# Kernel tuning notes

Hardware: AMD Instinct MI355X
Metric: run time of the kernel (lower is better)

The kernel has to match this reference:

```python
import jax, jax.numpy as jnp
import numpy as np

B, N, D_NET = 16, 2048, 64
L_SFC, D_VNF = 16, 32
HID, NHEAD, DFF, NLAYERS = 128, 4, 8, 2
NUM_NODES = 1024
SEQ = L_SFC + 2
EPS = 1e-5


def setup_inputs() -> dict:
    key = jax.random.key(0)
    ks = iter(jax.random.split(key, 40))
    def nrm(shape, scale=0.02):
        return (jax.random.normal(next(ks), shape, dtype=jnp.float32) * scale)
    inp = {
        'net_state': jax.random.normal(next(ks), (B, N, D_NET), dtype=jnp.float32),
        'sfc_state': jax.random.normal(next(ks), (B, L_SFC, D_VNF), dtype=jnp.float32),
        'node_pair': jax.random.randint(next(ks), (B, 2), 0, NUM_NODES),
        # manual attention projections (torch Linear layout [out,in])
        'Wq': nrm((4 * D_NET, D_NET)), 'bq': jnp.zeros((4 * D_NET,), jnp.float32),
        'Wk': nrm((4 * D_NET, D_NET)), 'bk': jnp.zeros((4 * D_NET,), jnp.float32),
        'Wv': nrm((4 * D_NET, D_NET)), 'bv': jnp.zeros((4 * D_NET,), jnp.float32),
        'net_W': nrm((HID, 4 * D_NET)), 'net_b': jnp.zeros((HID,), jnp.float32),
        'node_embed': nrm((NUM_NODES, D_VNF), 1.0),
        'sfc_W': nrm((HID, D_VNF)), 'sfc_b': jnp.zeros((HID,), jnp.float32),
        'pos_embed': nrm((SEQ, HID), 1.0),
        # 2 TransformerEncoderLayers, stacked on leading axis
        'qkv_w': nrm((NLAYERS, 3 * HID, HID)), 'qkv_b': jnp.zeros((NLAYERS, 3 * HID), jnp.float32),
        'out_w': nrm((NLAYERS, HID, HID)), 'out_b': jnp.zeros((NLAYERS, HID), jnp.float32),
        'ln1_w': jnp.ones((NLAYERS, HID), jnp.float32), 'ln1_b': jnp.zeros((NLAYERS, HID), jnp.float32),
        'lin1_w': nrm((NLAYERS, DFF, HID)), 'lin1_b': jnp.zeros((NLAYERS, DFF), jnp.float32),
        'lin2_w': nrm((NLAYERS, HID, DFF)), 'lin2_b': jnp.zeros((NLAYERS, HID), jnp.float32),
        'ln2_w': jnp.ones((NLAYERS, HID), jnp.float32), 'ln2_b': jnp.zeros((NLAYERS, HID), jnp.float32),
    }
    return inp


def _layernorm(x, w, b):
    mu = jnp.mean(x, axis=-1, keepdims=True)
    var = jnp.mean(jnp.square(x - mu), axis=-1, keepdims=True)
    return (x - mu) * jax.lax.rsqrt(var + EPS) * w + b


def _mha(x, w_qkv, b_qkv, w_out, b_out, pad_mask):
    Bx, S, H = x.shape
    hd = H // NHEAD
    qkv = x @ w_qkv.T + b_qkv                      # [B,S,3H]
    q, k, v = jnp.split(qkv, 3, axis=-1)
    q = q.reshape(Bx, S, NHEAD, hd).transpose(0, 2, 1, 3)
    k = k.reshape(Bx, S, NHEAD, hd).transpose(0, 2, 1, 3)
    v = v.reshape(Bx, S, NHEAD, hd).transpose(0, 2, 1, 3)
    scores = jnp.einsum('bhqd,bhkd->bhqk', q, k) / jnp.float32(hd) ** 0.5
    scores = scores + jnp.where(pad_mask[:, None, None, :], -1e9, 0.0)
    attn = jax.nn.softmax(scores, axis=-1)
    o = jnp.einsum('bhqk,bhkd->bhqd', attn, v).transpose(0, 2, 1, 3).reshape(Bx, S, H)
    return o @ w_out.T + b_out


def reference(net_state, sfc_state, node_pair, Wq, bq, Wk, bk, Wv, bv,
              net_W, net_b, node_embed, sfc_W, sfc_b, pos_embed,
              qkv_w, qkv_b, out_w, out_b, ln1_w, ln1_b,
              lin1_w, lin1_b, lin2_w, lin2_b, ln2_w, ln2_b):
    # --- net branch: manual single-head self-attention over nodes ---
    Q = net_state @ Wq.T + bq                       # [B,N,4D]
    K = net_state @ Wk.T + bk
    V = net_state @ Wv.T + bv
    scores = jnp.einsum('bnd,bmd->bnm', Q, K) / jnp.float32(net_state.shape[-1]) ** 0.5
    net_out = jax.nn.softmax(scores, axis=-1) @ V   # [B,N,4D]
    net_out = net_out @ net_W.T + net_b             # [B,N,HID]
    # --- sfc branch ---
    pair_emb = node_embed[node_pair]                # [B,2,D_VNF]
    sfc = jnp.concatenate([pair_emb[:, :1], sfc_state, pair_emb[:, 1:2]], axis=1)
    pad_mask = jnp.sum(jnp.abs(sfc), axis=-1) == 0  # [B,SEQ]
    x = sfc @ sfc_W.T + sfc_b + pos_embed[None, :sfc.shape[1]]
    for l in range(NLAYERS):  # post-norm TransformerEncoderLayer, relu, dropout=0
        x = _layernorm(x + _mha(x, qkv_w[l], qkv_b[l], out_w[l], out_b[l], pad_mask), ln1_w[l], ln1_b[l])
        ff = jax.nn.relu(x @ lin1_w[l].T + lin1_b[l]) @ lin2_w[l].T + lin2_b[l]
        x = _layernorm(x + ff, ln2_w[l], ln2_b[l])
    return jnp.concatenate([net_out, x], axis=1)    # [B, N+SEQ, HID]
```

## Files before the change

### kernel.cpp

```cpp
#include <hip/hip_runtime.h>
#include <cstdint>
#include <cstddef>

#define B_   16
#define N_   2048
#define DN   64
#define DQ   256
#define HID_ 128
#define SEQ_ 18
#define OUTR 2066
#define KVB  32

typedef __attribute__((ext_vector_type(4)))  float f32x4;
typedef __attribute__((ext_vector_type(16))) float f32x16;
typedef __attribute__((ext_vector_type(8)))  short bf16x8;

__device__ __forceinline__ unsigned cvtpk(float lo, float hi) {
  unsigned w;
  asm("v_cvt_pk_bf16_f32 %0, %1, %2" : "=v"(w) : "v"(lo), "v"(hi));
  return w;
}
__device__ __forceinline__ short f2bf(float f) {
  union { float f; unsigned u; } v; v.f = f;
  unsigned r = v.u + 0x7fffu + ((v.u >> 16) & 1u);
  return (short)(r >> 16);
}
__device__ __forceinline__ bf16x8 cvt8(const float* p) {
  f32x4 a = *(const f32x4*)p, b = *(const f32x4*)(p + 4);
  union { unsigned u[4]; bf16x8 v; } r;
  r.u[0] = cvtpk(a[0], a[1]); r.u[1] = cvtpk(a[2], a[3]);
  r.u[2] = cvtpk(b[0], b[1]); r.u[3] = cvtpk(b[2], b[3]);
  return r.v;
}
__device__ __forceinline__ float hadd4(f32x4 v) { return (v[0] + v[1]) + (v[2] + v[3]); }

__device__ __forceinline__ bf16x8 mkfrag(unsigned wa, unsigned wb,
                                         unsigned wc, unsigned wd, bool hi) {
  unsigned sa = (unsigned)__shfl_xor((int)wa, 32);
  unsigned sb = (unsigned)__shfl_xor((int)wb, 32);
  unsigned sc = (unsigned)__shfl_xor((int)wc, 32);
  unsigned sd = (unsigned)__shfl_xor((int)wd, 32);
  union { unsigned u[4]; bf16x8 v; } r;
  r.u[0] = hi ? sc : wa;
  r.u[1] = hi ? sd : wb;
  r.u[2] = hi ? wc : sa;
  r.u[3] = hi ? wd : sb;
  return r.v;
}

__global__ __launch_bounds__(512) void proj_kernel(
    const float* __restrict__ net, const float* __restrict__ Wq, const float* __restrict__ bq,
    const float* __restrict__ Wk, const float* __restrict__ bk,
    const float* __restrict__ Wv, const float* __restrict__ bv,
    const float* __restrict__ netW,
    short* __restrict__ Qb, short* __restrict__ Kb, short* __restrict__ Gf) {
  __shared__ char psm[98304];
  short* wl = (short*)psm;
  char* vrm = psm + 32768;

  const int gid = blockIdx.x;
  const int b = gid >> 4;
  const int r0 = (gid & 15) * 128;
  const int t = threadIdx.x;
  const int w = t >> 6, lane = t & 63, ln = lane & 15, g = lane >> 4;
  const int rw = r0 + w * 16;
  const int xk = (ln & 7) << 4;

  bf16x8 af[2];
#pragma unroll
  for (int c = 0; c < 2; ++c)
    af[c] = cvt8(net + ((size_t)b * N_ + rw + ln) * DN + c * 32 + g * 8);

  const float* Ws[3] = {Wq, Wk, Wv};
  for (int m = 0; m < 3; ++m) {
    __syncthreads();
#pragma unroll
    for (int it = 0; it < 8; ++it) {
      int idx = it * 512 + t;
      int row = idx >> 4, c8 = idx & 15;
      f32x4 v = *(const f32x4*)(Ws[m] + row * 64 + c8 * 4);
      int byo = row * 128 + ((c8 * 8) ^ ((row & 7) << 4));
      *(uint2*)((char*)wl + byo) = make_uint2(cvtpk(v[0], v[1]), cvtpk(v[2], v[3]));
    }
    __syncthreads();
    if (m < 2) {
      const float* bias = (m == 0) ? bq : bk;
      short* dst = (m == 0) ? Qb : Kb;
      const float sc = (m == 0) ? 0.125f : 1.0f;
#pragma unroll
      for (int tt = 0; tt < 16; ++tt) {
        f32x4 acc = {0.f, 0.f, 0.f, 0.f};
#pragma unroll
        for (int c = 0; c < 2; ++c) {
          int byo = (tt * 16 + ln) * 128 + ((c * 64 + g * 16) ^ xk);
          bf16x8 wf = *(const bf16x8*)((char*)wl + byo);
          acc = __builtin_amdgcn_mfma_f32_16x16x32_bf16(wf, af[c], acc, 0, 0, 0);
        }
        f32x4 b4 = *(const f32x4*)(bias + tt * 16 + g * 4);
        uint2 u = make_uint2(cvtpk((acc[0] + b4[0]) * sc, (acc[1] + b4[1]) * sc),
                             cvtpk((acc[2] + b4[2]) * sc, (acc[3] + b4[3]) * sc));
        *(uint2*)(dst + ((size_t)b * N_ + rw + ln) * DQ + tt * 16 + g * 4) = u;
      }
    } else {
#pragma unroll
      for (int tt = 0; tt < 16; ++tt) {
        f32x4 acc = {0.f, 0.f, 0.f, 0.f};
#pragma unroll
        for (int c = 0; c < 2; ++c) {
          int byo = (tt * 16 + ln) * 128 + ((c * 64 + g * 16) ^ xk);
          bf16x8 wf = *(const bf16x8*)((char*)wl + byo);
          acc = __builtin_amdgcn_mfma_f32_16x16x32_bf16(af[c], wf, acc, 0, 0, 0);
        }
        float bias = bv[tt * 16 + ln];
        int d = tt * 16 + ln;
#pragma unroll
        for (int r = 0; r < 4; ++r) {
          int nn = w * 16 + g * 4 + r;
          int byte = nn * 512 + ((d * 2) ^ ((nn & 7) << 4));
          *(short*)(vrm + byte) = f2bf(acc[r] + bias);
        }
      }
    }
  }
  __syncthreads();

  const int l31 = lane & 31, h = lane >> 5;
  const bool hb = (h != 0);
#pragma unroll
  for (int j = 0; j < 2; ++j) {
    int ti = w * 2 + j;
    int nt = ti >> 2, dt = ti & 3;
    f32x16 C;
#pragma unroll
    for (int r = 0; r < 16; ++r) C[r] = 0.f;
    int n = nt * 32 + l31;
#pragma unroll
    for (int dc = 0; dc < 16; ++dc) {
      bf16x8 A = *(const bf16x8*)(vrm + n * 512 + ((dc * 32 + h * 16) ^ ((n & 7) << 4)));
      bf16x8 Bf = cvt8(netW + (size_t)(dt * 32 + l31) * DQ + dc * 16 + h * 8);
      C = __builtin_amdgcn_mfma_f32_32x32x16_bf16(A, Bf, C, 0, 0, 0);
    }
    unsigned a0 = cvtpk(C[0],  C[1]),  a1 = cvtpk(C[2],  C[3]);
    unsigned a2 = cvtpk(C[4],  C[5]),  a3 = cvtpk(C[6],  C[7]);
    unsigned a4 = cvtpk(C[8],  C[9]),  a5 = cvtpk(C[10], C[11]);
    unsigned a6 = cvtpk(C[12], C[13]), a7 = cvtpk(C[14], C[15]);
    bf16x8 f0 = mkfrag(a0, a1, a2, a3, hb);
    bf16x8 f1 = mkfrag(a4, a5, a6, a7, hb);
    size_t base = (((size_t)b * 64 + (r0 >> 5) + nt) * 8 + dt * 2) * 512;
    *(bf16x8*)(Gf + base + lane * 8)       = f0;
    *(bf16x8*)(Gf + base + 512 + lane * 8) = f1;
  }
}

struct SfcS {
  float xs[SEQ_][132];
  float qkv[SEQ_][388];
  float scs[4][SEQ_][19];
  float sinb[SEQ_][32];
  float ffh[SEQ_][8];
  float maskv[SEQ_];
  short xbf[32 * 128];
};

__device__ __forceinline__ void par_ln(SfcS& S, const float* __restrict__ lw,
                                       const float* __restrict__ lb, int w, int lane) {
  float w0 = lw[lane * 2], w1 = lw[lane * 2 + 1];
  float b0 = lb[lane * 2], b1 = lb[lane * 2 + 1];
  for (int r = w; r < SEQ_; r += 8) {
    float2 v = *(const float2*)&S.qkv[r][128 + lane * 2];
    float s1 = v.x + v.y;
    float s2 = v.x * v.x + v.y * v.y;
#pragma unroll
    for (int off = 1; off < 64; off <<= 1) {
      s1 += __shfl_xor(s1, off);
      s2 += __shfl_xor(s2, off);
    }
    float mu = s1 * 0.0078125f;
    float var = s2 * 0.0078125f - mu * mu;
    float rsd = rsqrtf(var + 1e-5f);
    S.xs[r][lane * 2]     = (v.x - mu) * rsd * w0 + b0;
    S.xs[r][lane * 2 + 1] = (v.y - mu) * rsd * w1 + b1;
  }
}

__device__ __forceinline__ void rows_to_bf(const float* __restrict__ src, int stride,
                                           char* __restrict__ xbf, int t) {
  for (int i = t; i < SEQ_ * 16; i += 512) {
    int row = i >> 4, c8 = i & 15;
    const float* p = src + row * stride + c8 * 8;
    f32x4 a = *(const f32x4*)p;
    f32x4 b = *(const f32x4*)(p + 4);
    uint4 u;
    u.x = cvtpk(a[0], a[1]); u.y = cvtpk(a[2], a[3]);
    u.z = cvtpk(b[0], b[1]); u.w = cvtpk(b[2], b[3]);
    int byo = row * 256 + ((c8 * 16) ^ ((row & 7) << 4));
    *(uint4*)(xbf + byo) = u;
  }
}

__device__ void sfc_body(
    int b, SfcS& S,
    const float* __restrict__ sfc_state, const int* __restrict__ node_pair,
    const float* __restrict__ node_embed, const float* __restrict__ sfcW,
    const float* __restrict__ sfcb, const float* __restrict__ pos,
    const float* __restrict__ qkvW, const float* __restrict__ qkvB,
    const float* __restrict__ outW, const float* __restrict__ outB,
    const float* __restrict__ ln1w, const float* __restrict__ ln1b,
    const float* __restrict__ l1w, const float* __restrict__ l1b,
    const float* __restrict__ l2w, const float* __restrict__ l2b,
    const float* __restrict__ ln2w, const float* __restrict__ ln2b,
    float* __restrict__ out) {
  const int t = threadIdx.x;
  const int w = t >> 6, lane = t & 63, ln = lane & 15, g = lane >> 4;
  char* xbf = (char*)S.xbf;
  const int xk2 = (ln & 7) << 4;

  ((uint4*)xbf)[t] = make_uint4(0, 0, 0, 0);

  for (int i = t; i < SEQ_ * 32; i += 512) {
    int s = i >> 5, d = i & 31;
    float v;
    if (s == 0)       v = node_embed[node_pair[b * 2 + 0] * 32 + d];
    else if (s == 17) v = node_embed[node_pair[b * 2 + 1] * 32 + d];
    else              v = sfc_state[((size_t)b * 16 + (s - 1)) * 32 + d];
    S.sinb[s][d] = v;
  }
  __syncthreads();
  if (t < SEQ_) {
    float sum = 0.f;
#pragma unroll
    for (int d = 0; d < 32; ++d) sum += fabsf(S.sinb[t][d]);
    S.maskv[t] = (sum == 0.f) ? -1e9f : 0.f;
  }
  {
    int hh = t & 127, part = t >> 7;
    f32x4 wr[8];
#pragma unroll
    for (int j = 0; j < 8; ++j) wr[j] = *(const f32x4*)(sfcW + hh * 32 + j * 4);
    for (int si = part; si < SEQ_; si += 4) {
      f32x4 a = {0.f, 0.f, 0.f, 0.f};
#pragma unroll
      for (int j = 0; j < 8; ++j) a += wr[j] * (*(const f32x4*)&S.sinb[si][j * 4]);
      S.xs[si][hh] = hadd4(a) + sfcb[hh] + pos[si * HID_ + hh];
    }
  }
  __syncthreads();

  for (int ll = 0; ll < 2; ++ll) {
    rows_to_bf(&S.xs[0][0], 132, xbf, t);
    __syncthreads();
    if (t < 256) {
      bf16x8 af[2][4];
#pragma unroll
      for (int m = 0; m < 2; ++m)
#pragma unroll
        for (int k = 0; k < 4; ++k)
          af[m][k] = *(const bf16x8*)(xbf + (m * 16 + ln) * 256 + ((k * 64 + g * 16) ^ xk2));
#pragma unroll
      for (int i = 0; i < 6; ++i) {
        int nt = w + i * 4;
        const float* wp = qkvW + ((size_t)ll * 384 + nt * 16 + ln) * HID_;
        f32x4 a0 = {0.f, 0.f, 0.f, 0.f}, a1 = {0.f, 0.f, 0.f, 0.f};
#pragma unroll
        for (int k = 0; k < 4; ++k) {
          bf16x8 wf = cvt8(wp + k * 32 + g * 8);
          a0 = __builtin_amdgcn_mfma_f32_16x16x32_bf16(wf, af[0][k], a0, 0, 0, 0);
          a1 = __builtin_amdgcn_mfma_f32_16x16x32_bf16(wf, af[1][k], a1, 0, 0, 0);
        }
        f32x4 b4 = *(const f32x4*)(qkvB + ll * 384 + nt * 16 + g * 4);
#pragma unroll
        for (int r = 0; r < 4; ++r) {
          S.qkv[ln][nt * 16 + g * 4 + r] = a0[r] + b4[r];
          if (ln < 2) S.qkv[16 + ln][nt * 16 + g * 4 + r] = a1[r] + b4[r];
        }
      }
    }
    __syncthreads();
    for (int i = t; i < 4 * SEQ_ * SEQ_; i += 512) {
      int hh = i / (SEQ_ * SEQ_), rem = i - hh * SEQ_ * SEQ_;
      int qi = rem / SEQ_, kj = rem - qi * SEQ_;
      f32x4 a = {0.f, 0.f, 0.f, 0.f};
#pragma unroll
      for (int j = 0; j < 8; ++j)
        a += (*(const f32x4*)&S.qkv[qi][hh * 32 + j * 4]) *
             (*(const f32x4*)&S.qkv[kj][128 + hh * 32 + j * 4]);
      S.scs[hh][qi][kj] = hadd4(a) * 0.17677669529663687f + S.maskv[kj];
    }
    __syncthreads();
    if (t < 4 * SEQ_) {
      int hh = t / SEQ_, qi = t - hh * SEQ_;
      float mx = -1e30f;
#pragma unroll
      for (int j = 0; j < SEQ_; ++j) mx = fmaxf(mx, S.scs[hh][qi][j]);
      float sum = 0.f;
#pragma unroll
      for (int j = 0; j < SEQ_; ++j) {
        float e = __expf(S.scs[hh][qi][j] - mx);
        S.scs[hh][qi][j] = e; sum += e;
      }
      float inv = 1.f / sum;
#pragma unroll
      for (int j = 0; j < SEQ_; ++j) S.scs[hh][qi][j] *= inv;
    }
    __syncthreads();
    for (int i = t; i < SEQ_ * HID_; i += 512) {
      int s = i >> 7, hd = i & 127, hh = hd >> 5;
      float a = 0.f;
#pragma unroll
      for (int j = 0; j < SEQ_; ++j) a += S.scs[hh][s][j] * S.qkv[j][256 + hd];
      S.qkv[s][hd] = a;
    }
    __syncthreads();
    rows_to_bf(&S.qkv[0][0], 388, xbf, t);
    __syncthreads();
    if (t < 256) {
      bf16x8 af[2][4];
#pragma unroll
      for (int m = 0; m < 2; ++m)
#pragma unroll
        for (int k = 0; k < 4; ++k)
          af[m][k] = *(const bf16x8*)(xbf + (m * 16 + ln) * 256 + ((k * 64 + g * 16) ^ xk2));
#pragma unroll
      for (int i = 0; i < 2; ++i) {
        int nt = w + i * 4;
        const float* wp = outW + ((size_t)ll * HID_ + nt * 16 + ln) * HID_;
        f32x4 a0 = {0.f, 0.f, 0.f, 0.f}, a1 = {0.f, 0.f, 0.f, 0.f};
#pragma unroll
        for (int k = 0; k < 4; ++k) {
          bf16x8 wf = cvt8(wp + k * 32 + g * 8);
          a0 = __builtin_amdgcn_mfma_f32_16x16x32_bf16(wf, af[0][k], a0, 0, 0, 0);
          a1 = __builtin_amdgcn_mfma_f32_16x16x32_bf16(wf, af[1][k], a1, 0, 0, 0);
        }
        f32x4 b4 = *(const f32x4*)(outB + ll * HID_ + nt * 16 + g * 4);
#pragma unroll
        for (int r = 0; r < 4; ++r) {
          int h = nt * 16 + g * 4 + r;
          S.qkv[ln][128 + h] = S.xs[ln][h] + a0[r] + b4[r];
          if (ln < 2) S.qkv[16 + ln][128 + h] = S.xs[16 + ln][h] + a1[r] + b4[r];
        }
      }
    }
    __syncthreads();
    par_ln(S, ln1w + ll * HID_, ln1b + ll * HID_, w, lane);
    __syncthreads();
    if (t < SEQ_ * 8) {
      int s = t >> 3, oo = t & 7;
      const float* wp = l1w + ((size_t)ll * 8 + oo) * HID_;
      f32x4 a = {0.f, 0.f, 0.f, 0.f};
#pragma unroll
      for (int j = 0; j < 32; ++j)
        a += (*(const f32x4*)(wp + j * 4)) * (*(const f32x4*)&S.xs[s][j * 4]);
      S.ffh[s][oo] = fmaxf(hadd4(a) + l1b[ll * 8 + oo], 0.f);
    }
    __syncthreads();
    for (int i = t; i < SEQ_ * HID_; i += 512) {
      int s = i >> 7, h2 = i & 127;
      const float* wp = l2w + ((size_t)ll * HID_ + h2) * 8;
      float a = 0.f;
#pragma unroll
      for (int j = 0; j < 8; ++j) a += wp[j] * S.ffh[s][j];
      S.qkv[s][128 + h2] = S.xs[s][h2] + a + l2b[ll * HID_ + h2];
    }
    __syncthreads();
    par_ln(S, ln2w + ll * HID_, ln2b + ll * HID_, w, lane);
    __syncthreads();
  }
  for (int i = t; i < SEQ_ * HID_; i += 512) {
    int s = i >> 7, h2 = i & 127;
    out[((size_t)b * OUTR + 2048 + s) * HID_ + h2] = S.xs[s][h2];
  }
}

union ASmem { alignas(16) char attn[66048]; SfcS sfc; };

__global__ __launch_bounds__(512, 2) void attn_sfc_kernel(
    const short* __restrict__ Qb, const short* __restrict__ Kb,
    const short* __restrict__ Gf, const float* __restrict__ netb,
    const float* __restrict__ sfc_state, const int* __restrict__ node_pair,
    const float* __restrict__ node_embed, const float* __restrict__ sfcW,
    const float* __restrict__ sfcb, const float* __restrict__ pos,
    const float* __restrict__ qkvW, const float* __restrict__ qkvB,
    const float* __restrict__ outW, const float* __restrict__ outB,
    const float* __restrict__ ln1w, const float* __restrict__ ln1b,
    const float* __restrict__ l1w, const float* __restrict__ l1b,
    const float* __restrict__ l2w, const float* __restrict__ l2b,
    const float* __restrict__ ln2w, const float* __restrict__ ln2b,
    float* __restrict__ out) {
  __shared__ ASmem sm;
  if (blockIdx.x < 16) {
    sfc_body(blockIdx.x, sm.sfc, sfc_state, node_pair, node_embed, sfcW, sfcb, pos,
             qkvW, qkvB, outW, outB, ln1w, ln1b, l1w, l1b, l2w, l2b, ln2w, ln2b, out);
    return;
  }
  const int i = blockIdx.x - 16;
  const int b = (i & 7) * 2 + ((i >> 3) & 1);
  const int q0 = (i >> 4) * 128;
  const int t = threadIdx.x;
  const int w = t >> 6, l = t & 63;
  const int gr = w >> 2, wq = w & 3;
  const int l31 = l & 31, h = l >> 5, l7 = l & 7;
  const int qw = q0 + wq * 32;
  const bool hb = (h != 0);

  const short* Kg = Kb + ((size_t)b * N_ + (size_t)gr * 1024) * DQ;
  char* kb0 = sm.attn + gr * 32768;
  char* kb1 = kb0 + 16384;

  bf16x8 qf[16];
  const short* Qrow = Qb + ((size_t)b * N_ + qw + l31) * DQ + h * 8;
#pragma unroll
  for (int kc = 0; kc < 16; ++kc)
    qf[kc] = *(const bf16x8*)(Qrow + kc * 16);

  f32x16 o[4];
#pragma unroll
  for (int dt = 0; dt < 4; ++dt)
#pragma unroll
    for (int r = 0; r < 16; ++r) o[dt][r] = 0.f;
  float lsum = 0.f;

  auto stage_k = [&](int tile, char* dst) {
#pragma unroll
    for (int it = 0; it < 4; ++it) {
      int idx = wq * 4 + it;
      int row = idx * 2 + h;
      int gcol = (l31 * 16) ^ ((row & 7) << 4);
      const char* src = (const char*)(Kg + (size_t)(tile * KVB + row) * DQ) + gcol;
      __builtin_amdgcn_global_load_lds(
          (const __attribute__((address_space(1))) void*)src,
          (__attribute__((address_space(3))) void*)(dst + idx * 1024), 16, 0, 0);
    }
  };

  stage_k(0, kb0);
  __syncthreads();

  const short* Gb = Gf + (size_t)b * 64 * 4096;
  for (int tt = 0; tt < 32; ++tt) {
    char* kc_ = (tt & 1) ? kb1 : kb0;
    if (tt < 31) stage_k(tt + 1, (tt & 1) ? kb0 : kb1);
    const short* gt = Gb + (size_t)(gr * 32 + tt) * 4096 + l * 8;
    bf16x8 vw[8];
#pragma unroll
    for (int f = 0; f < 8; ++f)
      vw[f] = *(const bf16x8*)(gt + f * 512);
    f32x16 s;
#pragma unroll
    for (int r = 0; r < 16; ++r) s[r] = 0.f;
    __builtin_amdgcn_s_setprio(1);
#pragma unroll
    for (int kc = 0; kc < 16; ++kc) {
      bf16x8 kf = *(const bf16x8*)(kc_ + l31 * 512 + ((kc * 32 + h * 16) ^ (l7 << 4)));
      s = __builtin_amdgcn_mfma_f32_32x32x16_bf16(kf, qf[kc], s, 0, 0, 0);
    }
    __builtin_amdgcn_s_setprio(0);
#pragma unroll
    for (int r = 0; r < 16; ++r) { s[r] = __expf(s[r]); lsum += s[r]; }
    unsigned wA = cvtpk(s[0], s[1]),   wB = cvtpk(s[2], s[3]);
    unsigned wC = cvtpk(s[4], s[5]),   wD = cvtpk(s[6], s[7]);
    unsigned wE = cvtpk(s[8], s[9]),   wF = cvtpk(s[10], s[11]);
    unsigned wG = cvtpk(s[12], s[13]), wH = cvtpk(s[14], s[15]);
    bf16x8 pf0 = mkfrag(wA, wB, wC, wD, hb);
    bf16x8 pf1 = mkfrag(wE, wF, wG, wH, hb);
    __builtin_amdgcn_s_setprio(1);
#pragma unroll
    for (int dt = 0; dt < 4; ++dt) {
      o[dt] = __builtin_amdgcn_mfma_f32_32x32x16_bf16(vw[dt * 2],     pf0, o[dt], 0, 0, 0);
      o[dt] = __builtin_amdgcn_mfma_f32_32x32x16_bf16(vw[dt * 2 + 1], pf1, o[dt], 0, 0, 0);
    }
    __builtin_amdgcn_s_setprio(0);
    __syncthreads();
  }

  lsum += __shfl_xor(lsum, 32);

  float* lsums = (float*)(sm.attn + 65536);
  if (w >= 4) {
    char* base = sm.attn + (w - 4) * 16384;
#pragma unroll
    for (int dt = 0; dt < 4; ++dt)
#pragma unroll
      for (int rq = 0; rq < 4; ++rq) {
        f32x4 v;
        v[0] = o[dt][rq * 4 + 0]; v[1] = o[dt][rq * 4 + 1];
        v[2] = o[dt][rq * 4 + 2]; v[3] = o[dt][rq * 4 + 3];
        *(f32x4*)(base + ((dt * 4 + rq) * 64 + l) * 16) = v;
      }
    if (l < 32) lsums[(w - 4) * 32 + l31] = lsum;
  }
  __syncthreads();
  if (w < 4) {
    const char* base = sm.attn + w * 16384;
#pragma unroll
    for (int dt = 0; dt < 4; ++dt)
#pragma unroll
      for (int rq = 0; rq < 4; ++rq) {
        f32x4 v = *(const f32x4*)(base + ((dt * 4 + rq) * 64 + l) * 16);
        o[dt][rq * 4 + 0] += v[0]; o[dt][rq * 4 + 1] += v[1];
        o[dt][rq * 4 + 2] += v[2]; o[dt][rq * 4 + 3] += v[3];
      }
    const float ltot = lsum + lsums[w * 32 + l31];
    const float linv = 1.f / ltot;
    float* orow = out + ((size_t)b * OUTR + qw + l31) * HID_;
#pragma unroll
    for (int dt = 0; dt < 4; ++dt) {
#pragma unroll
      for (int rq = 0; rq < 4; ++rq) {
        f32x4 bia = *(const f32x4*)(netb + dt * 32 + rq * 8 + h * 4);
        f32x4 vv;
        vv[0] = o[dt][4 * rq + 0] * linv + bia[0];
        vv[1] = o[dt][4 * rq + 1] * linv + bia[1];
        vv[2] = o[dt][4 * rq + 2] * linv + bia[2];
        vv[3] = o[dt][4 * rq + 3] * linv + bia[3];
        *(f32x4*)(orow + dt * 32 + rq * 8 + h * 4) = vv;
      }
    }
  }
}

extern "C" void kernel_launch(void* const* d_in, const int* in_sizes, int n_in,
                              void* d_out, int out_size, void* d_ws, size_t ws_size,
                              hipStream_t stream) {
  (void)in_sizes; (void)n_in; (void)out_size; (void)ws_size;
  const float* net_state  = (const float*)d_in[0];
  const float* sfc_state  = (const float*)d_in[1];
  const int*   node_pair  = (const int*)d_in[2];
  const float* Wq   = (const float*)d_in[3];
  const float* bq   = (const float*)d_in[4];
  const float* Wk   = (const float*)d_in[5];
  const float* bk   = (const float*)d_in[6];
  const float* Wv   = (const float*)d_in[7];
  const float* bv   = (const float*)d_in[8];
  const float* netW = (const float*)d_in[9];
  const float* netb = (const float*)d_in[10];
  const float* node_embed = (const float*)d_in[11];
  const float* sfcW = (const float*)d_in[12];
  const float* sfcb = (const float*)d_in[13];
  const float* pos  = (const float*)d_in[14];
  const float* qkvW = (const float*)d_in[15];
  const float* qkvB = (const float*)d_in[16];
  const float* outW = (const float*)d_in[17];
  const float* outB = (const float*)d_in[18];
  const float* ln1w = (const float*)d_in[19];
  const float* ln1b = (const float*)d_in[20];
  const float* l1w  = (const float*)d_in[21];
  const float* l1b  = (const float*)d_in[22];
  const float* l2w  = (const float*)d_in[23];
  const float* l2b  = (const float*)d_in[24];
  const float* ln2w = (const float*)d_in[25];
  const float* ln2b = (const float*)d_in[26];
  float* out = (float*)d_out;

  const size_t S = (size_t)B_ * N_ * DQ;
  short* Qb = (short*)d_ws;
  short* Kb = Qb + S;
  short* Gf = Kb + S;

  proj_kernel<<<256, 512, 0, stream>>>(net_state, Wq, bq, Wk, bk, Wv, bv, netW, Qb, Kb, Gf);
  attn_sfc_kernel<<<272, 512, 0, stream>>>(Qb, Kb, Gf, netb,
                                           sfc_state, node_pair, node_embed, sfcW, sfcb, pos,
                                           qkvW, qkvB, outW, outB, ln1w, ln1b, l1w, l1b,
                                           l2w, l2b, ln2w, ln2b, out);
}
```

Baseline: 143.3 us.

## Run SFC transformer branch one batch per wave with global scratch

The SFC encoder branch now runs one batch element per wavefront instead of one per 512-thread block. Its state lives in a per-batch global-memory scratch region rather than shared memory, so the branch needs only 2 blocks instead of 16 and all block-level barriers are removed. The attention blocks are unchanged but now start earlier in the grid. In exchange, each wave does 8x more serial work and goes through cached global memory instead of LDS, which could lengthen the SFC critical path. That path runs concurrently with the attention blocks.

New measurement: 433.6 us. +202.5%, slower.

```diff
diff --git a/kernel.cpp b/kernel.cpp
--- a/kernel.cpp
+++ b/kernel.cpp
@@ -10,6 +10,7 @@
 #define SEQ_ 18
 #define OUTR 2066
 #define KVB  32
+#define SCR  18432
 
 typedef __attribute__((ext_vector_type(4)))  float f32x4;
 typedef __attribute__((ext_vector_type(16))) float f32x16;
@@ -152,54 +153,8 @@
   }
 }
 
-struct SfcS {
-  float xs[SEQ_][132];
-  float qkv[SEQ_][388];
-  float scs[4][SEQ_][19];
-  float sinb[SEQ_][32];
-  float ffh[SEQ_][8];
-  float maskv[SEQ_];
-  short xbf[32 * 128];
-};
-
-__device__ __forceinline__ void par_ln(SfcS& S, const float* __restrict__ lw,
-                                       const float* __restrict__ lb, int w, int lane) {
-  float w0 = lw[lane * 2], w1 = lw[lane * 2 + 1];
-  float b0 = lb[lane * 2], b1 = lb[lane * 2 + 1];
-  for (int r = w; r < SEQ_; r += 8) {
-    float2 v = *(const float2*)&S.qkv[r][128 + lane * 2];
-    float s1 = v.x + v.y;
-    float s2 = v.x * v.x + v.y * v.y;
-#pragma unroll
-    for (int off = 1; off < 64; off <<= 1) {
-      s1 += __shfl_xor(s1, off);
-      s2 += __shfl_xor(s2, off);
-    }
-    float mu = s1 * 0.0078125f;
-    float var = s2 * 0.0078125f - mu * mu;
-    float rsd = rsqrtf(var + 1e-5f);
-    S.xs[r][lane * 2]     = (v.x - mu) * rsd * w0 + b0;
-    S.xs[r][lane * 2 + 1] = (v.y - mu) * rsd * w1 + b1;
-  }
-}
-
-__device__ __forceinline__ void rows_to_bf(const float* __restrict__ src, int stride,
-                                           char* __restrict__ xbf, int t) {
-  for (int i = t; i < SEQ_ * 16; i += 512) {
-    int row = i >> 4, c8 = i & 15;
-    const float* p = src + row * stride + c8 * 8;
-    f32x4 a = *(const f32x4*)p;
-    f32x4 b = *(const f32x4*)(p + 4);
-    uint4 u;
-    u.x = cvtpk(a[0], a[1]); u.y = cvtpk(a[2], a[3]);
-    u.z = cvtpk(b[0], b[1]); u.w = cvtpk(b[2], b[3]);
-    int byo = row * 256 + ((c8 * 16) ^ ((row & 7) << 4));
-    *(uint4*)(xbf + byo) = u;
-  }
-}
-
-__device__ void sfc_body(
-    int b, SfcS& S,
+__device__ void sfc_wave(
+    int b, float* g,
     const float* __restrict__ sfc_state, const int* __restrict__ node_pair,
     const float* __restrict__ node_embed, const float* __restrict__ sfcW,
     const float* __restrict__ sfcb, const float* __restrict__ pos,
@@ -210,172 +165,206 @@
     const float* __restrict__ l2w, const float* __restrict__ l2b,
     const float* __restrict__ ln2w, const float* __restrict__ ln2b,
     float* __restrict__ out) {
-  const int t = threadIdx.x;
-  const int w = t >> 6, lane = t & 63, ln = lane & 15, g = lane >> 4;
-  char* xbf = (char*)S.xbf;
-  const int xk2 = (ln & 7) << 4;
-
-  ((uint4*)xbf)[t] = make_uint4(0, 0, 0, 0);
-
-  for (int i = t; i < SEQ_ * 32; i += 512) {
+  const int lane = threadIdx.x & 63;
+  const int ln = lane & 15, g8 = lane >> 4;
+  float* xp = g;
+  float* qk = g + 4224;
+  float* ap = g + 11208;
+  float* sc = g + 15432;
+  float* sb = g + 16800;
+  float* ff = g + 17376;
+  float* mv = g + 17520;
+
+  for (int i = lane; i < 1056; i += 64) {
+    ((f32x4*)xp)[i] = (f32x4){0.f, 0.f, 0.f, 0.f};
+    ((f32x4*)ap)[i] = (f32x4){0.f, 0.f, 0.f, 0.f};
+  }
+  for (int i = lane; i < 576; i += 64) {
     int s = i >> 5, d = i & 31;
     float v;
     if (s == 0)       v = node_embed[node_pair[b * 2 + 0] * 32 + d];
     else if (s == 17) v = node_embed[node_pair[b * 2 + 1] * 32 + d];
     else              v = sfc_state[((size_t)b * 16 + (s - 1)) * 32 + d];
-    S.sinb[s][d] = v;
-  }
-  __syncthreads();
-  if (t < SEQ_) {
+    sb[i] = v;
+  }
+  if (lane < SEQ_) {
     float sum = 0.f;
 #pragma unroll
-    for (int d = 0; d < 32; ++d) sum += fabsf(S.sinb[t][d]);
-    S.maskv[t] = (sum == 0.f) ? -1e9f : 0.f;
-  }
-  {
-    int hh = t & 127, part = t >> 7;
+    for (int d = 0; d < 32; ++d) sum += fabsf(sb[lane * 32 + d]);
+    mv[lane] = (sum == 0.f) ? -1e9f : 0.f;
+  }
+#pragma unroll
+  for (int ch = 0; ch < 2; ++ch) {
+    int hh = ch * 64 + lane;
     f32x4 wr[8];
 #pragma unroll
     for (int j = 0; j < 8; ++j) wr[j] = *(const f32x4*)(sfcW + hh * 32 + j * 4);
-    for (int si = part; si < SEQ_; si += 4) {
+    for (int si = 0; si < SEQ_; ++si) {
       f32x4 a = {0.f, 0.f, 0.f, 0.f};
 #pragma unroll
-      for (int j = 0; j < 8; ++j) a += wr[j] * (*(const f32x4*)&S.sinb[si][j * 4]);
-      S.xs[si][hh] = hadd4(a) + sfcb[hh] + pos[si * HID_ + hh];
-    }
-  }
-  __syncthreads();
+      for (int j = 0; j < 8; ++j) a += wr[j] * (*(const f32x4*)&sb[si * 32 + j * 4]);
+      xp[si * 132 + hh] = hadd4(a) + sfcb[hh] + pos[si * HID_ + hh];
+    }
+  }
 
   for (int ll = 0; ll < 2; ++ll) {
-    rows_to_bf(&S.xs[0][0], 132, xbf, t);
-    __syncthreads();
-    if (t < 256) {
-      bf16x8 af[2][4];
-#pragma unroll
-      for (int m = 0; m < 2; ++m)
-#pragma unroll
-        for (int k = 0; k < 4; ++k)
-          af[m][k] = *(const bf16x8*)(xbf + (m * 16 + ln) * 256 + ((k * 64 + g * 16) ^ xk2));
-#pragma unroll
-      for (int i = 0; i < 6; ++i) {
-        int nt = w + i * 4;
+    {
+      bf16x8 af0[4], af1[4];
+#pragma unroll
+      for (int k = 0; k < 4; ++k) {
+        af0[k] = cvt8(xp + ln * 132 + k * 32 + g8 * 8);
+        af1[k] = cvt8(xp + (16 + ln) * 132 + k * 32 + g8 * 8);
+      }
+      for (int nt = 0; nt < 24; ++nt) {
         const float* wp = qkvW + ((size_t)ll * 384 + nt * 16 + ln) * HID_;
         f32x4 a0 = {0.f, 0.f, 0.f, 0.f}, a1 = {0.f, 0.f, 0.f, 0.f};
 #pragma unroll
         for (int k = 0; k < 4; ++k) {
-          bf16x8 wf = cvt8(wp + k * 32 + g * 8);
-          a0 = __builtin_amdgcn_mfma_f32_16x16x32_bf16(wf, af[0][k], a0, 0, 0, 0);
-          a1 = __builtin_amdgcn_mfma_f32_16x16x32_bf16(wf, af[1][k], a1, 0, 0, 0);
-        }
-        f32x4 b4 = *(const f32x4*)(qkvB + ll * 384 + nt * 16 + g * 4);
+          bf16x8 wf = cvt8(wp + k * 32 + g8 * 8);
+          a0 = __builtin_amdgcn_mfma_f32_16x16x32_bf16(wf, af0[k], a0, 0, 0, 0);
+          a1 = __builtin_amdgcn_mfma_f32_16x16x32_bf16(wf, af1[k], a1, 0, 0, 0);
+        }
+        f32x4 b4 = *(const f32x4*)(qkvB + ll * 384 + nt * 16 + g8 * 4);
 #pragma unroll
         for (int r = 0; r < 4; ++r) {
-          S.qkv[ln][nt * 16 + g * 4 + r] = a0[r] + b4[r];
-          if (ln < 2) S.qkv[16 + ln][nt * 16 + g * 4 + r] = a1[r] + b4[r];
-        }
-      }
-    }
-    __syncthreads();
-    for (int i = t; i < 4 * SEQ_ * SEQ_; i += 512) {
-      int hh = i / (SEQ_ * SEQ_), rem = i - hh * SEQ_ * SEQ_;
-      int qi = rem / SEQ_, kj = rem - qi * SEQ_;
-      f32x4 a = {0.f, 0.f, 0.f, 0.f};
-#pragma unroll
-      for (int j = 0; j < 8; ++j)
-        a += (*(const f32x4*)&S.qkv[qi][hh * 32 + j * 4]) *
-             (*(const f32x4*)&S.qkv[kj][128 + hh * 32 + j * 4]);
-      S.scs[hh][qi][kj] = hadd4(a) * 0.17677669529663687f + S.maskv[kj];
-    }
-    __syncthreads();
-    if (t < 4 * SEQ_) {
-      int hh = t / SEQ_, qi = t - hh * SEQ_;
-      float mx = -1e30f;
-#pragma unroll
-      for (int j = 0; j < SEQ_; ++j) mx = fmaxf(mx, S.scs[hh][qi][j]);
-      float sum = 0.f;
-#pragma unroll
-      for (int j = 0; j < SEQ_; ++j) {
-        float e = __expf(S.scs[hh][qi][j] - mx);
-        S.scs[hh][qi][j] = e; sum += e;
-      }
-      float inv = 1.f / sum;
-#pragma unroll
-      for (int j = 0; j < SEQ_; ++j) S.scs[hh][qi][j] *= inv;
-    }
-    __syncthreads();
-    for (int i = t; i < SEQ_ * HID_; i += 512) {
+          qk[ln * 388 + nt * 16 + g8 * 4 + r] = a0[r] + b4[r];
+          if (ln < 2) qk[(16 + ln) * 388 + nt * 16 + g8 * 4 + r] = a1[r] + b4[r];
+        }
+      }
+    }
+    for (int base = 0; base < 1296; base += 64) {
+      int i = base + lane;
+      if (i < 1296) {
+        int hh = i / 324, rem = i - hh * 324;
+        int qi = rem / SEQ_, kj = rem - qi * SEQ_;
+        f32x4 a = {0.f, 0.f, 0.f, 0.f};
+#pragma unroll
+        for (int j = 0; j < 8; ++j)
+          a += (*(const f32x4*)&qk[qi * 388 + hh * 32 + j * 4]) *
+               (*(const f32x4*)&qk[kj * 388 + 128 + hh * 32 + j * 4]);
+        sc[(hh * SEQ_ + qi) * 19 + kj] = hadd4(a) * 0.17677669529663687f + mv[kj];
+      }
+    }
+    for (int base = 0; base < 72; base += 64) {
+      int i = base + lane;
+      if (i < 72) {
+        int hh = i / SEQ_, qi = i - hh * SEQ_;
+        float* row = sc + (hh * SEQ_ + qi) * 19;
+        float mx = -1e30f;
+#pragma unroll
+        for (int j = 0; j < SEQ_; ++j) mx = fmaxf(mx, row[j]);
+        float sum = 0.f;
+#pragma unroll
+        for (int j = 0; j < SEQ_; ++j) {
+          float e = __expf(row[j] - mx);
+          row[j] = e; sum += e;
+        }
+        float inv = 1.f / sum;
+#pragma unroll
+        for (int j = 0; j < SEQ_; ++j) row[j] *= inv;
+      }
+    }
+    for (int i = lane; i < SEQ_ * HID_; i += 64) {
       int s = i >> 7, hd = i & 127, hh = hd >> 5;
       float a = 0.f;
 #pragma unroll
-      for (int j = 0; j < SEQ_; ++j) a += S.scs[hh][s][j] * S.qkv[j][256 + hd];
-      S.qkv[s][hd] = a;
-    }
-    __syncthreads();
-    rows_to_bf(&S.qkv[0][0], 388, xbf, t);
-    __syncthreads();
-    if (t < 256) {
-      bf16x8 af[2][4];
-#pragma unroll
-      for (int m = 0; m < 2; ++m)
-#pragma unroll
-        for (int k = 0; k < 4; ++k)
-          af[m][k] = *(const bf16x8*)(xbf + (m * 16 + ln) * 256 + ((k * 64 + g * 16) ^ xk2));
-#pragma unroll
-      for (int i = 0; i < 2; ++i) {
-        int nt = w + i * 4;
+      for (int j = 0; j < SEQ_; ++j) a += sc[(hh * SEQ_ + s) * 19 + j] * qk[j * 388 + 256 + hd];
+      ap[s * 132 + hd] = a;
+    }
+    {
+      bf16x8 af0[4], af1[4];
+#pragma unroll
+      for (int k = 0; k < 4; ++k) {
+        af0[k] = cvt8(ap + ln * 132 + k * 32 + g8 * 8);
+        af1[k] = cvt8(ap + (16 + ln) * 132 + k * 32 + g8 * 8);
+      }
+      for (int nt = 0; nt < 8; ++nt) {
         const float* wp = outW + ((size_t)ll * HID_ + nt * 16 + ln) * HID_;
         f32x4 a0 = {0.f, 0.f, 0.f, 0.f}, a1 = {0.f, 0.f, 0.f, 0.f};
 #pragma unroll
         for (int k = 0; k < 4; ++k) {
-          bf16x8 wf = cvt8(wp + k * 32 + g * 8);
-          a0 = __builtin_amdgcn_mfma_f32_16x16x32_bf16(wf, af[0][k], a0, 0, 0, 0);
-          a1 = __builtin_amdgcn_mfma_f32_16x16x32_bf16(wf, af[1][k], a1, 0, 0, 0);
-        }
-        f32x4 b4 = *(const f32x4*)(outB + ll * HID_ + nt * 16 + g * 4);
+          bf16x8 wf = cvt8(wp + k * 32 + g8 * 8);
+          a0 = __builtin_amdgcn_mfma_f32_16x16x32_bf16(wf, af0[k], a0, 0, 0, 0);
+          a1 = __builtin_amdgcn_mfma_f32_16x16x32_bf16(wf, af1[k], a1, 0, 0, 0);
+        }
+        f32x4 b4 = *(const f32x4*)(outB + ll * HID_ + nt * 16 + g8 * 4);
 #pragma unroll
         for (int r = 0; r < 4; ++r) {
-          int h = nt * 16 + g * 4 + r;
-          S.qkv[ln][128 + h] = S.xs[ln][h] + a0[r] + b4[r];
-          if (ln < 2) S.qkv[16 + ln][128 + h] = S.xs[16 + ln][h] + a1[r] + b4[r];
-        }
-      }
-    }
-    __syncthreads();
-    par_ln(S, ln1w + ll * HID_, ln1b + ll * HID_, w, lane);
-    __syncthreads();
-    if (t < SEQ_ * 8) {
-      int s = t >> 3, oo = t & 7;
-      const float* wp = l1w + ((size_t)ll * 8 + oo) * HID_;
-      f32x4 a = {0.f, 0.f, 0.f, 0.f};
-#pragma unroll
-      for (int j = 0; j < 32; ++j)
-        a += (*(const f32x4*)(wp + j * 4)) * (*(const f32x4*)&S.xs[s][j * 4]);
-      S.ffh[s][oo] = fmaxf(hadd4(a) + l1b[ll * 8 + oo], 0.f);
-    }
-    __syncthreads();
-    for (int i = t; i < SEQ_ * HID_; i += 512) {
+          int h = nt * 16 + g8 * 4 + r;
+          qk[ln * 388 + 128 + h] = xp[ln * 132 + h] + a0[r] + b4[r];
+          if (ln < 2) qk[(16 + ln) * 388 + 128 + h] = xp[(16 + ln) * 132 + h] + a1[r] + b4[r];
+        }
+      }
+    }
+    {
+      const float* lw = ln1w + ll * HID_; const float* lb = ln1b + ll * HID_;
+      float w0 = lw[lane * 2], w1 = lw[lane * 2 + 1];
+      float b0 = lb[lane * 2], b1 = lb[lane * 2 + 1];
+      for (int r = 0; r < SEQ_; ++r) {
+        float2 v = *(const float2*)&qk[r * 388 + 128 + lane * 2];
+        float s1 = v.x + v.y, s2 = v.x * v.x + v.y * v.y;
+#pragma unroll
+        for (int off = 1; off < 64; off <<= 1) {
+          s1 += __shfl_xor(s1, off);
+          s2 += __shfl_xor(s2, off);
+        }
+        float mu = s1 * 0.0078125f;
+        float var = s2 * 0.0078125f - mu * mu;
+        float rsd = rsqrtf(var + 1e-5f);
+        xp[r * 132 + lane * 2]     = (v.x - mu) * rsd * w0 + b0;
+        xp[r * 132 + lane * 2 + 1] = (v.y - mu) * rsd * w1 + b1;
+      }
+    }
+    for (int base = 0; base < 144; base += 64) {
+      int i = base + lane;
+      if (i < 144) {
+        int s = i >> 3, oo = i & 7;
+        const float* wp = l1w + ((size_t)ll * 8 + oo) * HID_;
+        f32x4 a = {0.f, 0.f, 0.f, 0.f};
+#pragma unroll
+        for (int j = 0; j < 32; ++j)
+          a += (*(const f32x4*)(wp + j * 4)) * (*(const f32x4*)&xp[s * 132 + j * 4]);
+        ff[s * 8 + oo] = fmaxf(hadd4(a) + l1b[ll * 8 + oo], 0.f);
+      }
+    }
+    for (int i = lane; i < SEQ_ * HID_; i += 64) {
       int s = i >> 7, h2 = i & 127;
       const float* wp = l2w + ((size_t)ll * HID_ + h2) * 8;
       float a = 0.f;
 #pragma unroll
-      for (int j = 0; j < 8; ++j) a += wp[j] * S.ffh[s][j];
-      S.qkv[s][128 + h2] = S.xs[s][h2] + a + l2b[ll * HID_ + h2];
-    }
-    __syncthreads();
-    par_ln(S, ln2w + ll * HID_, ln2b + ll * HID_, w, lane);
-    __syncthreads();
-  }
-  for (int i = t; i < SEQ_ * HID_; i += 512) {
+      for (int j = 0; j < 8; ++j) a += wp[j] * ff[s * 8 + j];
+      qk[s * 388 + 128 + h2] = xp[s * 132 + h2] + a + l2b[ll * HID_ + h2];
+    }
+    {
+      const float* lw = ln2w + ll * HID_; const float* lb = ln2b + ll * HID_;
+      float w0 = lw[lane * 2], w1 = lw[lane * 2 + 1];
+      float b0 = lb[lane * 2], b1 = lb[lane * 2 + 1];
+      for (int r = 0; r < SEQ_; ++r) {
+        float2 v = *(const float2*)&qk[r * 388 + 128 + lane * 2];
+        float s1 = v.x + v.y, s2 = v.x * v.x + v.y * v.y;
+#pragma unroll
+        for (int off = 1; off < 64; off <<= 1) {
+          s1 += __shfl_xor(s1, off);
+          s2 += __shfl_xor(s2, off);
+        }
+        float mu = s1 * 0.0078125f;
+        float var = s2 * 0.0078125f - mu * mu;
+        float rsd = rsqrtf(var + 1e-5f);
+        xp[r * 132 + lane * 2]     = (v.x - mu) * rsd * w0 + b0;
+        xp[r * 132 + lane * 2 + 1] = (v.y - mu) * rsd * w1 + b1;
+      }
+    }
+  }
+  for (int i = lane; i < SEQ_ * HID_; i += 64) {
     int s = i >> 7, h2 = i & 127;
-    out[((size_t)b * OUTR + 2048 + s) * HID_ + h2] = S.xs[s][h2];
-  }
-}
-
-union ASmem { alignas(16) char attn[66048]; SfcS sfc; };
+    out[((size_t)b * OUTR + 2048 + s) * HID_ + h2] = xp[s * 132 + h2];
+  }
+}
 
 __global__ __launch_bounds__(512, 2) void attn_sfc_kernel(
     const short* __restrict__ Qb, const short* __restrict__ Kb,
     const short* __restrict__ Gf, const float* __restrict__ netb,
+    float* Sg,
     const float* __restrict__ sfc_state, const int* __restrict__ node_pair,
     const float* __restrict__ node_embed, const float* __restrict__ sfcW,
     const float* __restrict__ sfcb, const float* __restrict__ pos,
@@ -386,13 +375,14 @@
     const float* __restrict__ l2w, const float* __restrict__ l2b,
     const float* __restrict__ ln2w, const float* __restrict__ ln2b,
     float* __restrict__ out) {
-  __shared__ ASmem sm;
-  if (blockIdx.x < 16) {
-    sfc_body(blockIdx.x, sm.sfc, sfc_state, node_pair, node_embed, sfcW, sfcb, pos,
+  __shared__ char smattn[66048];
+  if (blockIdx.x < 2) {
+    int b = blockIdx.x * 8 + (threadIdx.x >> 6);
+    sfc_wave(b, Sg + (size_t)b * SCR, sfc_state, node_pair, node_embed, sfcW, sfcb, pos,
              qkvW, qkvB, outW, outB, ln1w, ln1b, l1w, l1b, l2w, l2b, ln2w, ln2b, out);
     return;
   }
-  const int i = blockIdx.x - 16;
+  const int i = blockIdx.x - 2;
   const int b = (i & 7) * 2 + ((i >> 3) & 1);
   const int q0 = (i >> 4) * 128;
   const int t = threadIdx.x;
@@ -403,7 +393,7 @@
   const bool hb = (h != 0);
 
   const short* Kg = Kb + ((size_t)b * N_ + (size_t)gr * 1024) * DQ;
-  char* kb0 = sm.attn + gr * 32768;
+  char* kb0 = smattn + gr * 32768;
   char* kb1 = kb0 + 16384;
 
   bf16x8 qf[16];
@@ -474,9 +464,9 @@
 
   lsum += __shfl_xor(lsum, 32);
 
-  float* lsums = (float*)(sm.attn + 65536);
+  float* lsums = (float*)(smattn + 65536);
   if (w >= 4) {
-    char* base = sm.attn + (w - 4) * 16384;
+    char* base = smattn + (w - 4) * 16384;
 #pragma unroll
     for (int dt = 0; dt < 4; ++dt)
 #pragma unroll
@@ -490,7 +480,7 @@
   }
   __syncthreads();
   if (w < 4) {
-    const char* base = sm.attn + w * 16384;
+    const char* base = smattn + w * 16384;
 #pragma unroll
     for (int dt = 0; dt < 4; ++dt)
 #pragma unroll
@@ -555,9 +545,10 @@
   short* Qb = (short*)d_ws;
   short* Kb = Qb + S;
   short* Gf = Kb + S;
+  float* Sg = (float*)(Gf + (size_t)4194304);
 
   proj_kernel<<<256, 512, 0, stream>>>(net_state, Wq, bq, Wk, bk, Wv, bv, netW, Qb, Kb, Gf);
-  attn_sfc_kernel<<<272, 512, 0, stream>>>(Qb, Kb, Gf, netb,
+  attn_sfc_kernel<<<258, 512, 0, stream>>>(Qb, Kb, Gf, netb, Sg,
                                            sfc_state, node_pair, node_embed, sfcW, sfcb, pos,
                                            qkvW, qkvB, outW, outB, ln1w, ln1b, l1w, l1b,
                                            l2w, l2b, ln2w, ln2b, out);
```

## Give each wave one attention head in the SFC encoder to drop block barriers

Applied to the files above, without the earlier changes.

The SFC transformer work is rearranged so that wave w computes the Q, K and V tiles for head w, then that head's scores, softmax and probability-times-V, all without block-wide barriers in between. The output projection now uses all 8 waves with one tile each. LayerNorm, the FFN and the second LayerNorm run per wave on interleaved rows, so those stages need no barriers between them either. The goal is to cut the many __syncthreads along the short serial SFC path. The cost is that only 4 of the 8 waves work during most stages, and correctness depends on LDS ordering within a wave.

After: 147.2 us. 2.7% more time.

```diff
diff --git a/kernel.cpp b/kernel.cpp
--- a/kernel.cpp
+++ b/kernel.cpp
@@ -162,27 +162,6 @@
   short xbf[32 * 128];
 };
 
-__device__ __forceinline__ void par_ln(SfcS& S, const float* __restrict__ lw,
-                                       const float* __restrict__ lb, int w, int lane) {
-  float w0 = lw[lane * 2], w1 = lw[lane * 2 + 1];
-  float b0 = lb[lane * 2], b1 = lb[lane * 2 + 1];
-  for (int r = w; r < SEQ_; r += 8) {
-    float2 v = *(const float2*)&S.qkv[r][128 + lane * 2];
-    float s1 = v.x + v.y;
-    float s2 = v.x * v.x + v.y * v.y;
-#pragma unroll
-    for (int off = 1; off < 64; off <<= 1) {
-      s1 += __shfl_xor(s1, off);
-      s2 += __shfl_xor(s2, off);
-    }
-    float mu = s1 * 0.0078125f;
-    float var = s2 * 0.0078125f - mu * mu;
-    float rsd = rsqrtf(var + 1e-5f);
-    S.xs[r][lane * 2]     = (v.x - mu) * rsd * w0 + b0;
-    S.xs[r][lane * 2 + 1] = (v.y - mu) * rsd * w1 + b1;
-  }
-}
-
 __device__ __forceinline__ void rows_to_bf(const float* __restrict__ src, int stride,
                                            char* __restrict__ xbf, int t) {
   for (int i = t; i < SEQ_ * 16; i += 512) {
@@ -195,6 +174,27 @@
     u.z = cvtpk(b[0], b[1]); u.w = cvtpk(b[2], b[3]);
     int byo = row * 256 + ((c8 * 16) ^ ((row & 7) << 4));
     *(uint4*)(xbf + byo) = u;
+  }
+}
+
+__device__ __forceinline__ void par_ln(SfcS& S, const float* __restrict__ lw,
+                                       const float* __restrict__ lb, int w, int lane) {
+  float w0 = lw[lane * 2], w1 = lw[lane * 2 + 1];
+  float b0 = lb[lane * 2], b1 = lb[lane * 2 + 1];
+  for (int r = w; r < SEQ_; r += 4) {
+    float2 v = *(const float2*)&S.qkv[r][128 + lane * 2];
+    float s1 = v.x + v.y;
+    float s2 = v.x * v.x + v.y * v.y;
+#pragma unroll
+    for (int off = 1; off < 64; off <<= 1) {
+      s1 += __shfl_xor(s1, off);
+      s2 += __shfl_xor(s2, off);
+    }
+    float mu = s1 * 0.0078125f;
+    float var = s2 * 0.0078125f - mu * mu;
+    float rsd = rsqrtf(var + 1e-5f);
+    S.xs[r][lane * 2]     = (v.x - mu) * rsd * w0 + b0;
+    S.xs[r][lane * 2 + 1] = (v.y - mu) * rsd * w1 + b1;
   }
 }
 
@@ -249,23 +249,24 @@
   for (int ll = 0; ll < 2; ++ll) {
     rows_to_bf(&S.xs[0][0], 132, xbf, t);
     __syncthreads();
-    if (t < 256) {
-      bf16x8 af[2][4];
-#pragma unroll
-      for (int m = 0; m < 2; ++m)
-#pragma unroll
-        for (int k = 0; k < 4; ++k)
-          af[m][k] = *(const bf16x8*)(xbf + (m * 16 + ln) * 256 + ((k * 64 + g * 16) ^ xk2));
+    if (w < 4) {
+      bf16x8 af0[4], af1[4];
+#pragma unroll
+      for (int k = 0; k < 4; ++k) {
+        af0[k] = *(const bf16x8*)(xbf + ln * 256 + ((k * 64 + g * 16) ^ xk2));
+        af1[k] = *(const bf16x8*)(xbf + (16 + ln) * 256 + ((k * 64 + g * 16) ^ xk2));
+      }
+      const int ntl[6] = {2 * w, 2 * w + 1, 8 + 2 * w, 9 + 2 * w, 16 + 2 * w, 17 + 2 * w};
 #pragma unroll
       for (int i = 0; i < 6; ++i) {
-        int nt = w + i * 4;
+        int nt = ntl[i];
         const float* wp = qkvW + ((size_t)ll * 384 + nt * 16 + ln) * HID_;
         f32x4 a0 = {0.f, 0.f, 0.f, 0.f}, a1 = {0.f, 0.f, 0.f, 0.f};
 #pragma unroll
         for (int k = 0; k < 4; ++k) {
           bf16x8 wf = cvt8(wp + k * 32 + g * 8);
-          a0 = __builtin_amdgcn_mfma_f32_16x16x32_bf16(wf, af[0][k], a0, 0, 0, 0);
-          a1 = __builtin_amdgcn_mfma_f32_16x16x32_bf16(wf, af[1][k], a1, 0, 0, 0);
+          a0 = __builtin_amdgcn_mfma_f32_16x16x32_bf16(wf, af0[k], a0, 0, 0, 0);
+          a1 = __builtin_amdgcn_mfma_f32_16x16x32_bf16(wf, af1[k], a1, 0, 0, 0);
         }
         f32x4 b4 = *(const f32x4*)(qkvB + ll * 384 + nt * 16 + g * 4);
 #pragma unroll
@@ -274,95 +275,94 @@
           if (ln < 2) S.qkv[16 + ln][nt * 16 + g * 4 + r] = a1[r] + b4[r];
         }
       }
-    }
-    __syncthreads();
-    for (int i = t; i < 4 * SEQ_ * SEQ_; i += 512) {
-      int hh = i / (SEQ_ * SEQ_), rem = i - hh * SEQ_ * SEQ_;
-      int qi = rem / SEQ_, kj = rem - qi * SEQ_;
-      f32x4 a = {0.f, 0.f, 0.f, 0.f};
-#pragma unroll
-      for (int j = 0; j < 8; ++j)
-        a += (*(const f32x4*)&S.qkv[qi][hh * 32 + j * 4]) *
-             (*(const f32x4*)&S.qkv[kj][128 + hh * 32 + j * 4]);
-      S.scs[hh][qi][kj] = hadd4(a) * 0.17677669529663687f + S.maskv[kj];
-    }
-    __syncthreads();
-    if (t < 4 * SEQ_) {
-      int hh = t / SEQ_, qi = t - hh * SEQ_;
-      float mx = -1e30f;
-#pragma unroll
-      for (int j = 0; j < SEQ_; ++j) mx = fmaxf(mx, S.scs[hh][qi][j]);
-      float sum = 0.f;
-#pragma unroll
-      for (int j = 0; j < SEQ_; ++j) {
-        float e = __expf(S.scs[hh][qi][j] - mx);
-        S.scs[hh][qi][j] = e; sum += e;
-      }
-      float inv = 1.f / sum;
-#pragma unroll
-      for (int j = 0; j < SEQ_; ++j) S.scs[hh][qi][j] *= inv;
-    }
-    __syncthreads();
-    for (int i = t; i < SEQ_ * HID_; i += 512) {
-      int s = i >> 7, hd = i & 127, hh = hd >> 5;
-      float a = 0.f;
-#pragma unroll
-      for (int j = 0; j < SEQ_; ++j) a += S.scs[hh][s][j] * S.qkv[j][256 + hd];
-      S.qkv[s][hd] = a;
+      for (int i = lane; i < SEQ_ * SEQ_; i += 64) {
+        int qi = i / SEQ_, kj = i - qi * SEQ_;
+        f32x4 a = {0.f, 0.f, 0.f, 0.f};
+#pragma unroll
+        for (int j = 0; j < 8; ++j)
+          a += (*(const f32x4*)&S.qkv[qi][w * 32 + j * 4]) *
+               (*(const f32x4*)&S.qkv[kj][128 + w * 32 + j * 4]);
+        S.scs[w][qi][kj] = hadd4(a) * 0.17677669529663687f + S.maskv[kj];
+      }
+      if (lane < SEQ_) {
+        float* row = &S.scs[w][lane][0];
+        float mx = -1e30f;
+#pragma unroll
+        for (int j = 0; j < SEQ_; ++j) mx = fmaxf(mx, row[j]);
+        float sum = 0.f;
+#pragma unroll
+        for (int j = 0; j < SEQ_; ++j) {
+          float e = __expf(row[j] - mx);
+          row[j] = e; sum += e;
+        }
+        float inv = 1.f / sum;
+#pragma unroll
+        for (int j = 0; j < SEQ_; ++j) row[j] *= inv;
+      }
+      for (int i = lane; i < SEQ_ * 32; i += 64) {
+        int s = i >> 5, j = i & 31;
+        float a = 0.f;
+#pragma unroll
+        for (int jj = 0; jj < SEQ_; ++jj)
+          a += S.scs[w][s][jj] * S.qkv[jj][256 + w * 32 + j];
+        S.qkv[s][w * 32 + j] = a;
+      }
     }
     __syncthreads();
     rows_to_bf(&S.qkv[0][0], 388, xbf, t);
     __syncthreads();
-    if (t < 256) {
-      bf16x8 af[2][4];
-#pragma unroll
-      for (int m = 0; m < 2; ++m)
-#pragma unroll
-        for (int k = 0; k < 4; ++k)
-          af[m][k] = *(const bf16x8*)(xbf + (m * 16 + ln) * 256 + ((k * 64 + g * 16) ^ xk2));
-#pragma unroll
-      for (int i = 0; i < 2; ++i) {
-        int nt = w + i * 4;
-        const float* wp = outW + ((size_t)ll * HID_ + nt * 16 + ln) * HID_;
-        f32x4 a0 = {0.f, 0.f, 0.f, 0.f}, a1 = {0.f, 0.f, 0.f, 0.f};
-#pragma unroll
-        for (int k = 0; k < 4; ++k) {
-          bf16x8 wf = cvt8(wp + k * 32 + g * 8);
-          a0 = __builtin_amdgcn_mfma_f32_16x16x32_bf16(wf, af[0][k], a0, 0, 0, 0);
-          a1 = __builtin_amdgcn_mfma_f32_16x16x32_bf16(wf, af[1][k], a1, 0, 0, 0);
-        }
-        f32x4 b4 = *(const f32x4*)(outB + ll * HID_ + nt * 16 + g * 4);
-#pragma unroll
-        for (int r = 0; r < 4; ++r) {
-          int h = nt * 16 + g * 4 + r;
-          S.qkv[ln][128 + h] = S.xs[ln][h] + a0[r] + b4[r];
-          if (ln < 2) S.qkv[16 + ln][128 + h] = S.xs[16 + ln][h] + a1[r] + b4[r];
-        }
-      }
-    }
-    __syncthreads();
-    par_ln(S, ln1w + ll * HID_, ln1b + ll * HID_, w, lane);
-    __syncthreads();
-    if (t < SEQ_ * 8) {
-      int s = t >> 3, oo = t & 7;
-      const float* wp = l1w + ((size_t)ll * 8 + oo) * HID_;
-      f32x4 a = {0.f, 0.f, 0.f, 0.f};
-#pragma unroll
-      for (int j = 0; j < 32; ++j)
-        a += (*(const f32x4*)(wp + j * 4)) * (*(const f32x4*)&S.xs[s][j * 4]);
-      S.ffh[s][oo] = fmaxf(hadd4(a) + l1b[ll * 8 + oo], 0.f);
-    }
-    __syncthreads();
-    for (int i = t; i < SEQ_ * HID_; i += 512) {
-      int s = i >> 7, h2 = i & 127;
-      const float* wp = l2w + ((size_t)ll * HID_ + h2) * 8;
-      float a = 0.f;
-#pragma unroll
-      for (int j = 0; j < 8; ++j) a += wp[j] * S.ffh[s][j];
-      S.qkv[s][128 + h2] = S.xs[s][h2] + a + l2b[ll * HID_ + h2];
-    }
-    __syncthreads();
-    par_ln(S, ln2w + ll * HID_, ln2b + ll * HID_, w, lane);
+    {
+      bf16x8 af0[4], af1[4];
+#pragma unroll
+      for (int k = 0; k < 4; ++k) {
+        af0[k] = *(const bf16x8*)(xbf + ln * 256 + ((k * 64 + g * 16) ^ xk2));
+        af1[k] = *(const bf16x8*)(xbf + (16 + ln) * 256 + ((k * 64 + g * 16) ^ xk2));
+      }
+      const int nt = w;
+      const float* wp = outW + ((size_t)ll * HID_ + nt * 16 + ln) * HID_;
+      f32x4 a0 = {0.f, 0.f, 0.f, 0.f}, a1 = {0.f, 0.f, 0.f, 0.f};
+#pragma unroll
+      for (int k = 0; k < 4; ++k) {
+        bf16x8 wf = cvt8(wp + k * 32 + g * 8);
+        a0 = __builtin_amdgcn_mfma_f32_16x16x32_bf16(wf, af0[k], a0, 0, 0, 0);
+        a1 = __builtin_amdgcn_mfma_f32_16x16x32_bf16(wf, af1[k], a1, 0, 0, 0);
+      }
+      f32x4 b4 = *(const f32x4*)(outB + ll * HID_ + nt * 16 + g * 4);
+#pragma unroll
+      for (int r = 0; r < 4; ++r) {
+        int h = nt * 16 + g * 4 + r;
+        S.qkv[ln][128 + h] = S.xs[ln][h] + a0[r] + b4[r];
+        if (ln < 2) S.qkv[16 + ln][128 + h] = S.xs[16 + ln][h] + a1[r] + b4[r];
+      }
+    }
+    __syncthreads();
+    if (w < 4) {
+      par_ln(S, ln1w + ll * HID_, ln1b + ll * HID_, w, lane);
+      if (lane < 40) {
+        int rr = lane >> 3, oo = lane & 7;
+        int s = w + rr * 4;
+        if (s < SEQ_) {
+          const float* wp = l1w + ((size_t)ll * 8 + oo) * HID_;
+          f32x4 a = {0.f, 0.f, 0.f, 0.f};
+#pragma unroll
+          for (int j = 0; j < 32; ++j)
+            a += (*(const f32x4*)(wp + j * 4)) * (*(const f32x4*)&S.xs[s][j * 4]);
+          S.ffh[s][oo] = fmaxf(hadd4(a) + l1b[ll * 8 + oo], 0.f);
+        }
+      }
+      for (int i = lane; i < 5 * HID_; i += 64) {
+        int rr = i >> 7, h2 = i & 127;
+        int s = w + rr * 4;
+        if (s < SEQ_) {
+          const float* wp = l2w + ((size_t)ll * HID_ + h2) * 8;
+          float a = 0.f;
+#pragma unroll
+          for (int j = 0; j < 8; ++j) a += wp[j] * S.ffh[s][j];
+          S.qkv[s][128 + h2] = S.xs[s][h2] + a + l2b[ll * HID_ + h2];
+        }
+      }
+      par_ln(S, ln2w + ll * HID_, ln2b + ll * HID_, w, lane);
+    }
     __syncthreads();
   }
   for (int i = t; i < SEQ_ * HID_; i += 512) {
```
